# Kernel optimization log

Hardware: AMD Instinct MI355X
Metric: run time of the kernel (lower is better)

The kernel has to match this reference:

```python
import jax, jax.numpy as jnp
import numpy as np
import math

B, S, D = 2, 2048, 1024
H = 16
DK = D // H  # dim_k == dim_v == 64


def setup_inputs() -> dict:
    key = jax.random.key(0)
    ks = jax.random.split(key, 8)
    scale = 1.0 / math.sqrt(D)
    inp = {
        "query": jax.random.normal(ks[0], (B, S, D), dtype=jnp.float32),
        "key": jax.random.normal(ks[1], (B, S, D), dtype=jnp.float32),
        "value": jax.random.normal(ks[2], (B, S, D), dtype=jnp.float32),
        # stacked per-head projection weights (torch Linear y = x @ W.T; here stored as [H, D, DK])
        "Wq": jax.random.uniform(ks[3], (H, D, DK), dtype=jnp.float32, minval=-scale, maxval=scale),
        "Wk": jax.random.uniform(ks[4], (H, D, DK), dtype=jnp.float32, minval=-scale, maxval=scale),
        "Wv": jax.random.uniform(ks[5], (H, D, DK), dtype=jnp.float32, minval=-scale, maxval=scale),
        "Wo": jax.random.uniform(ks[6], (D, H * DK), dtype=jnp.float32, minval=-scale, maxval=scale),
        "bo": jax.random.uniform(ks[7], (D,), dtype=jnp.float32, minval=-scale, maxval=scale),
    }
    return inp


def reference(query, key, value, Wq, Wk, Wv, Wo, bo):
    # per-head projections, batched over heads via einsum
    q = jnp.einsum("bsd,hdk->bhsk", query, Wq)   # [B,H,S,DK]
    k = jnp.einsum("btd,hdk->bhtk", key, Wk)     # [B,H,S,DK]
    v = jnp.einsum("btd,hdv->bhtv", value, Wv)   # [B,H,S,DK]
    scores = jnp.einsum("bhsk,bhtk->bhst", q, k) / jnp.sqrt(jnp.float32(DK))
    # causal mask (is_causal=True): strictly upper triangle -> -inf
    causal = jnp.tril(jnp.ones((S, S), dtype=bool))  # True = keep
    scores = jnp.where(causal[None, None], scores, -jnp.inf)
    attn = jax.nn.softmax(scores, axis=-1)
    # NaN correction (no-op under pure causal masking, kept for faithfulness)
    attn = jnp.where(jnp.isnan(attn), 0.0, attn)
    out = jnp.einsum("bhst,bhtv->bhsv", attn, v)  # [B,H,S,DK]
    out = jnp.transpose(out, (0, 2, 1, 3)).reshape(B, S, H * DK)  # concat heads
    return out @ Wo.T + bo
```

## Files before the change

kernel.cpp:

```cpp
#include <hip/hip_runtime.h>


#define B_ 2
#define S_ 2048
#define D_ 1024
#define H_ 16
#define DK_ 64
#define NEG_BIG (-1e30f)

typedef unsigned short u16;
typedef __attribute__((ext_vector_type(8))) short bf16x8;
typedef __attribute__((ext_vector_type(4))) float f32x4;

__device__ __forceinline__ float b2f(u16 v) {
    union { unsigned u; float f; } x; x.u = ((unsigned)v) << 16; return x.f;
}
__device__ __forceinline__ u16 f2b(float f) {
    union { float f; unsigned u; } x; x.f = f;
    unsigned r = x.u + 0x7fff + ((x.u >> 16) & 1);
    return (u16)(r >> 16);
}
__device__ __forceinline__ u16 f2b_fast(float f) {
    union { float f; unsigned u; } x; x.f = f;
    return (u16)((x.u + 0x8000u) >> 16);
}

__device__ __forceinline__ bool is_f32(const void* p) {
    const unsigned* u = (const unsigned*)p;
    int cnt = 0;
#pragma unroll
    for (int i = 0; i < 64; i++) {
        unsigned e = (u[i * 8] >> 7) & 0xFFu;
        cnt += (e >= 110u && e <= 134u) ? 1 : 0;
    }
    return cnt < 32;
}

template<bool F32>
__device__ __forceinline__ bf16x8 load8(const void* p, size_t idx) {
    if constexpr (F32) {
        const float* f = (const float*)p + idx;
        float4 a = *(const float4*)f;
        float4 b = *(const float4*)(f + 4);
        bf16x8 r;
        ((u16*)&r)[0] = f2b(a.x); ((u16*)&r)[1] = f2b(a.y);
        ((u16*)&r)[2] = f2b(a.z); ((u16*)&r)[3] = f2b(a.w);
        ((u16*)&r)[4] = f2b(b.x); ((u16*)&r)[5] = f2b(b.y);
        ((u16*)&r)[6] = f2b(b.z); ((u16*)&r)[7] = f2b(b.w);
        return r;
    } else {
        return *(const bf16x8*)((const u16*)p + idx);
    }
}

__global__ __launch_bounds__(256) void wtrans(const void* Wq, const void* Wk, const void* Wv,
                                              u16* WqT, u16* WkT, u16* WvT) {
    __shared__ __align__(16) u16 Ts[64][72];
    const int t = threadIdx.x;
    const int k0 = blockIdx.x * 64;
    const int h = blockIdx.y;
    const int wsel = blockIdx.z;
    const void* W = (wsel == 0) ? Wq : (wsel == 1) ? Wk : Wv;
    u16* WT = (wsel == 0) ? WqT : (wsel == 1) ? WkT : WvT;
    const bool wf = is_f32(W);

    const int drow = t >> 2, c0 = (t & 3) * 16;
    size_t sidx = ((size_t)h * D_ + k0 + drow) * DK_ + c0;
    bf16x8 v0, v1;
    if (wf) { v0 = load8<true >(W, sidx); v1 = load8<true >(W, sidx + 8); }
    else    { v0 = load8<false>(W, sidx); v1 = load8<false>(W, sidx + 8); }
    *(bf16x8*)&Ts[drow][c0]     = v0;
    *(bf16x8*)&Ts[drow][c0 + 8] = v1;
    __syncthreads();

    const int nrow = t >> 2, kc0 = (t & 3) * 16;
    u16 tmp[16];
#pragma unroll
    for (int j = 0; j < 16; j++) tmp[j] = Ts[kc0 + j][nrow];
    u16* dst = &WT[((size_t)h * DK_ + nrow) * D_ + k0 + kc0];
    *(bf16x8*)&dst[0] = *(const bf16x8*)&tmp[0];
    *(bf16x8*)&dst[8] = *(const bf16x8*)&tmp[8];
}

template<bool AF32>
__device__ void qproj_body(const void* A, const u16* WT, u16* Qt, int bb,
                           u16 (*As)[64][72], u16 (*Wt)[64][72]) {
    const int tid = threadIdx.x, mt = blockIdx.x, h = blockIdx.y;
    const int w = tid >> 6, lane = tid & 63, quad = lane >> 4, ln = lane & 15;
    const int s0 = mt * 64;
    const int row = tid >> 3, col = (tid & 7) * 8;
    const int row1 = row + 32;
    const int brow = tid >> 2, bc0 = (tid & 3) * 16;
    const size_t wbase = ((size_t)h * DK_ + brow) * D_ + bc0;

    bf16x8 areg0, areg1, breg0, breg1;
    areg0 = load8<AF32>(A, ((size_t)bb * S_ + s0 + row ) * D_ + col);
    areg1 = load8<AF32>(A, ((size_t)bb * S_ + s0 + row1) * D_ + col);
    breg0 = *(const bf16x8*)&WT[wbase];
    breg1 = *(const bf16x8*)&WT[wbase + 8];

    f32x4 acc[4];
#pragma unroll
    for (int t = 0; t < 4; t++)
#pragma unroll
        for (int r = 0; r < 4; r++) acc[t][r] = 0.f;

    int buf = 0;
    for (int k0 = 0; k0 < D_; k0 += 64, buf ^= 1) {
        *(bf16x8*)&As[buf][row ][col] = areg0;
        *(bf16x8*)&As[buf][row1][col] = areg1;
        *(bf16x8*)&Wt[buf][brow][bc0    ] = breg0;
        *(bf16x8*)&Wt[buf][brow][bc0 + 8] = breg1;
        __syncthreads();
        if (k0 + 64 < D_) {
            areg0 = load8<AF32>(A, ((size_t)bb * S_ + s0 + row ) * D_ + k0 + 64 + col);
            areg1 = load8<AF32>(A, ((size_t)bb * S_ + s0 + row1) * D_ + k0 + 64 + col);
            breg0 = *(const bf16x8*)&WT[wbase + k0 + 64];
            breg1 = *(const bf16x8*)&WT[wbase + k0 + 64 + 8];
        }
#pragma unroll
        for (int kk = 0; kk < 2; kk++) {
            bf16x8 a = *(const bf16x8*)&As[buf][w * 16 + ln][kk * 32 + quad * 8];
#pragma unroll
            for (int t = 0; t < 4; t++) {
                bf16x8 bm = *(const bf16x8*)&Wt[buf][t * 16 + ln][kk * 32 + quad * 8];
                acc[t] = __builtin_amdgcn_mfma_f32_16x16x32_bf16(a, bm, acc[t], 0, 0, 0);
            }
        }
    }

#pragma unroll
    for (int t = 0; t < 4; t++)
#pragma unroll
        for (int r = 0; r < 4; r++)
            Qt[((size_t)bb * S_ + s0 + w * 16 + quad * 4 + r) * D_ + h * DK_ + t * 16 + ln] =
                f2b(acc[t][r] * 0.125f);
}

__global__ __launch_bounds__(256) void qproj(const void* query, const u16* WqT, u16* Qt) {
    __shared__ __align__(16) u16 As[2][64][72];
    __shared__ __align__(16) u16 Wt[2][64][72];
    const int bb = blockIdx.z;
    if (is_f32(query)) qproj_body<true >(query, WqT, Qt, bb, As, Wt);
    else               qproj_body<false>(query, WqT, Qt, bb, As, Wt);
}

template<bool AF32>
__device__ void projkv_body(const void* A, const u16* WT, u16* Ko, u16* VTo,
                            int bb, int which, u16 (*As)[64][72], u16 (*Wt)[64][72]) {
    const int tid = threadIdx.x, mt = blockIdx.x, h = blockIdx.y;
    const int w = tid >> 6, lane = tid & 63, quad = lane >> 4, ln = lane & 15;
    const int s0 = mt * 64;
    const int row = tid >> 3, col = (tid & 7) * 8;
    const int row1 = row + 32;
    const int brow = tid >> 2, bc0 = (tid & 3) * 16;
    const size_t wbase = ((size_t)h * DK_ + brow) * D_ + bc0;

    bf16x8 areg0, areg1, breg0, breg1;
    areg0 = load8<AF32>(A, ((size_t)bb * S_ + s0 + row ) * D_ + col);
    areg1 = load8<AF32>(A, ((size_t)bb * S_ + s0 + row1) * D_ + col);
    breg0 = *(const bf16x8*)&WT[wbase];
    breg1 = *(const bf16x8*)&WT[wbase + 8];

    f32x4 acc[4];
#pragma unroll
    for (int t = 0; t < 4; t++)
#pragma unroll
        for (int r = 0; r < 4; r++) acc[t][r] = 0.f;

    int buf = 0;
    for (int k0 = 0; k0 < D_; k0 += 64, buf ^= 1) {
        *(bf16x8*)&As[buf][row ][col] = areg0;
        *(bf16x8*)&As[buf][row1][col] = areg1;
        *(bf16x8*)&Wt[buf][brow][bc0    ] = breg0;
        *(bf16x8*)&Wt[buf][brow][bc0 + 8] = breg1;
        __syncthreads();
        if (k0 + 64 < D_) {
            areg0 = load8<AF32>(A, ((size_t)bb * S_ + s0 + row ) * D_ + k0 + 64 + col);
            areg1 = load8<AF32>(A, ((size_t)bb * S_ + s0 + row1) * D_ + k0 + 64 + col);
            breg0 = *(const bf16x8*)&WT[wbase + k0 + 64];
            breg1 = *(const bf16x8*)&WT[wbase + k0 + 64 + 8];
        }
#pragma unroll
        for (int kk = 0; kk < 2; kk++) {
            bf16x8 a = *(const bf16x8*)&As[buf][w * 16 + ln][kk * 32 + quad * 8];
#pragma unroll
            for (int t = 0; t < 4; t++) {
                bf16x8 bm = *(const bf16x8*)&Wt[buf][t * 16 + ln][kk * 32 + quad * 8];
                acc[t] = __builtin_amdgcn_mfma_f32_16x16x32_bf16(a, bm, acc[t], 0, 0, 0);
            }
        }
    }

    if (which == 0) {
#pragma unroll
        for (int t = 0; t < 4; t++)
#pragma unroll
            for (int r = 0; r < 4; r++)
                Ko[((size_t)h * S_ + s0 + w * 16 + quad * 4 + r) * DK_ + t * 16 + ln] =
                    f2b(acc[t][r]);
    } else {
#pragma unroll
        for (int t = 0; t < 4; t++)
#pragma unroll
            for (int r = 0; r < 4; r++)
                Wt[0][t * 16 + ln][w * 16 + quad * 4 + r] = f2b(acc[t][r]);
        __syncthreads();
        *(bf16x8*)&VTo[((size_t)h * DK_ + row ) * S_ + s0 + col] = *(const bf16x8*)&Wt[0][row ][col];
        *(bf16x8*)&VTo[((size_t)h * DK_ + row1) * S_ + s0 + col] = *(const bf16x8*)&Wt[0][row1][col];
    }
}

__global__ __launch_bounds__(256) void projkv(const void* key, const void* value,
                                              const u16* WkT, const u16* WvT,
                                              u16* KVbase, int bb) {
    __shared__ __align__(16) u16 As[2][64][72];
    __shared__ __align__(16) u16 Wt[2][64][72];
    const int which = blockIdx.z;
    const void* A = which ? value : key;
    const u16* WT = which ? WvT : WkT;
    u16* Ko  = KVbase;
    u16* VTo = KVbase + (size_t)H_ * S_ * DK_;
    if (is_f32(A)) projkv_body<true >(A, WT, Ko, VTo, bb, which, As, Wt);
    else           projkv_body<false>(A, WT, Ko, VTo, bb, which, As, Wt);
}

__global__ __launch_bounds__(512) void flashq(u16* __restrict__ Xq,
                                              const u16* __restrict__ KV,
                                              int bb0, size_t zstride) {
    __shared__ __align__(16) u16 BufA[2][64][72];
    __shared__ __align__(16) u16 BufB[2][64][72];
    __shared__ __align__(16) u16 Ps[8][16][72];
    const int tid = threadIdx.x;
    const int bx = (int)blockIdx.x;
    const int qt = (blockIdx.z & 1) ? bx : ((int)gridDim.x - 1 - bx);
    const int h = blockIdx.y;
    const int bb = bb0 + blockIdx.z;
    const u16* Kb  = KV + (size_t)blockIdx.z * zstride;
    const u16* VTb = Kb + (size_t)H_ * S_ * DK_;
    const int w = tid >> 6, lane = tid & 63, quad = lane >> 4, ln = lane & 15;
    const int half = w >> 2, wr = w & 3;
    const int s0 = qt * 128;
    const int srow = tid >> 3, scol = (tid & 7) * 8;
    const int j0max = 2 * qt;
    const int jmax  = 2 * qt + 1;
    const int jdiag = half ? jmax : j0max;

    bf16x8 kreg = *(const bf16x8*)&Kb [((size_t)h * S_  + srow) * DK_ + scol];
    bf16x8 vreg = *(const bf16x8*)&VTb[((size_t)h * DK_ + srow) * S_  + scol];

    *(bf16x8*)&BufA[0][srow][scol] = *(const bf16x8*)&Xq[((size_t)bb * S_ + s0 + srow) * D_ + h * DK_ + scol];
    *(bf16x8*)&BufA[1][srow][scol] = *(const bf16x8*)&Xq[((size_t)bb * S_ + s0 + 64 + srow) * D_ + h * DK_ + scol];
    __syncthreads();
    bf16x8 qa0 = *(const bf16x8*)&BufA[half][wr * 16 + ln][quad * 8];
    bf16x8 qa1 = *(const bf16x8*)&BufA[half][wr * 16 + ln][32 + quad * 8];
    __syncthreads();

    f32x4 O[4];
    float psum[4];
#pragma unroll
    for (int t = 0; t < 4; t++)
#pragma unroll
        for (int r = 0; r < 4; r++) O[t][r] = 0.f;
#pragma unroll
    for (int r = 0; r < 4; r++) psum[r] = 0.f;

    for (int j = 0; j <= jmax; j++) {
        const int buf = j & 1;
        *(bf16x8*)&BufA[buf][srow][scol] = kreg;
        *(bf16x8*)&BufB[buf][srow][scol] = vreg;
        __syncthreads();

        if (j < jmax) {
            kreg = *(const bf16x8*)&Kb [((size_t)h * S_  + (j + 1) * 64 + srow) * DK_ + scol];
            vreg = *(const bf16x8*)&VTb[((size_t)h * DK_ + srow) * S_ + (j + 1) * 64 + scol];
        }

        const bool act = half ? true : (j <= j0max);

        if (act) {
            f32x4 sf[4];
#pragma unroll
            for (int t = 0; t < 4; t++)
#pragma unroll
                for (int r = 0; r < 4; r++) sf[t][r] = 0.f;
#pragma unroll
            for (int kk = 0; kk < 2; kk++) {
                bf16x8 a = kk ? qa1 : qa0;
#pragma unroll
                for (int t = 0; t < 4; t++) {
                    bf16x8 bm = *(const bf16x8*)&BufA[buf][t * 16 + ln][kk * 32 + quad * 8];
                    sf[t] = __builtin_amdgcn_mfma_f32_16x16x32_bf16(a, bm, sf[t], 0, 0, 0);
                }
            }
            if (j == jdiag) {
#pragma unroll
                for (int t = 0; t < 4; t++) {
                    int keyl = t * 16 + ln;
#pragma unroll
                    for (int r = 0; r < 4; r++) {
                        int qr = wr * 16 + quad * 4 + r;
                        if (keyl > qr) sf[t][r] = NEG_BIG;
                    }
                }
            }
#pragma unroll
            for (int t = 0; t < 4; t++)
#pragma unroll
                for (int r = 0; r < 4; r++) {
                    float p = __expf(sf[t][r]);
                    psum[r] += p;
                    Ps[w][quad * 4 + r][t * 16 + ln] = f2b_fast(p);
                }
        }
        __syncthreads();

        if (act) {
#pragma unroll
            for (int kk = 0; kk < 2; kk++) {
                bf16x8 a = *(const bf16x8*)&Ps[w][ln][kk * 32 + quad * 8];
#pragma unroll
                for (int t = 0; t < 4; t++) {
                    bf16x8 bm = *(const bf16x8*)&BufB[buf][t * 16 + ln][kk * 32 + quad * 8];
                    O[t] = __builtin_amdgcn_mfma_f32_16x16x32_bf16(a, bm, O[t], 0, 0, 0);
                }
            }
        }
    }

#pragma unroll
    for (int r = 0; r < 4; r++) {
        float s = psum[r];
        s += __shfl_xor(s, 1, 64);
        s += __shfl_xor(s, 2, 64);
        s += __shfl_xor(s, 4, 64);
        s += __shfl_xor(s, 8, 64);
        float inv = 1.0f / s;
        int sr = s0 + half * 64 + wr * 16 + quad * 4 + r;
#pragma unroll
        for (int t = 0; t < 4; t++) {
            Xq[((size_t)bb * S_ + sr) * D_ + h * DK_ + t * 16 + ln] = f2b(O[t][r] * inv);
        }
    }
}

__global__ __launch_bounds__(256) void copyx(const u16* __restrict__ src,
                                             u16* __restrict__ dst) {
    size_t i = ((size_t)blockIdx.x * 256 + threadIdx.x) * 8;
    *(bf16x8*)&dst[i] = *(const bf16x8*)&src[i];
}

template<bool WF32>
__device__ void outgemm_body(const u16* X, const void* Wo, const void* bo, bool bf32,
                             float* Y, u16 (*As)[64][72], u16 (*Bs)[64][72]) {
    const int tid = threadIdx.x, mt = blockIdx.x, nt = blockIdx.y;
    const int w = tid >> 6, lane = tid & 63, quad = lane >> 4, ln = lane & 15;
    const int m0 = mt * 64, n0 = nt * 64;
    const int row = tid >> 3, col = (tid & 7) * 8;
    const int row1 = row + 32;

    bf16x8 areg0, areg1, wreg0, wreg1;
    areg0 = *(const bf16x8*)&X[(size_t)(m0 + row ) * D_ + col];
    areg1 = *(const bf16x8*)&X[(size_t)(m0 + row1) * D_ + col];
    wreg0 = load8<WF32>(Wo, (size_t)(n0 + row ) * D_ + col);
    wreg1 = load8<WF32>(Wo, (size_t)(n0 + row1) * D_ + col);

    f32x4 acc[4];
#pragma unroll
    for (int t = 0; t < 4; t++)
#pragma unroll
        for (int r = 0; r < 4; r++) acc[t][r] = 0.f;

    int buf = 0;
    for (int k0 = 0; k0 < D_; k0 += 64, buf ^= 1) {
        *(bf16x8*)&As[buf][row ][col] = areg0;
        *(bf16x8*)&As[buf][row1][col] = areg1;
        *(bf16x8*)&Bs[buf][row ][col] = wreg0;
        *(bf16x8*)&Bs[buf][row1][col] = wreg1;
        __syncthreads();
        if (k0 + 64 < D_) {
            areg0 = *(const bf16x8*)&X[(size_t)(m0 + row ) * D_ + k0 + 64 + col];
            areg1 = *(const bf16x8*)&X[(size_t)(m0 + row1) * D_ + k0 + 64 + col];
            wreg0 = load8<WF32>(Wo, (size_t)(n0 + row ) * D_ + k0 + 64 + col);
            wreg1 = load8<WF32>(Wo, (size_t)(n0 + row1) * D_ + k0 + 64 + col);
        }
#pragma unroll
        for (int kk = 0; kk < 2; kk++) {
            bf16x8 a = *(const bf16x8*)&As[buf][w * 16 + ln][kk * 32 + quad * 8];
#pragma unroll
            for (int t = 0; t < 4; t++) {
                bf16x8 bm = *(const bf16x8*)&Bs[buf][t * 16 + ln][kk * 32 + quad * 8];
                acc[t] = __builtin_amdgcn_mfma_f32_16x16x32_bf16(a, bm, acc[t], 0, 0, 0);
            }
        }
    }

#pragma unroll
    for (int t = 0; t < 4; t++) {
        int n = n0 + t * 16 + ln;
        float bias = bf32 ? ((const float*)bo)[n] : b2f(((const u16*)bo)[n]);
#pragma unroll
        for (int r = 0; r < 4; r++) {
            int m = m0 + w * 16 + quad * 4 + r;
            Y[(size_t)m * D_ + n] = acc[t][r] + bias;
        }
    }
}

__global__ __launch_bounds__(256) void outgemm(const u16* __restrict__ X,
                                               const void* Wo, const void* bo,
                                               float* __restrict__ Y) {
    __shared__ __align__(16) u16 As[2][64][72];
    __shared__ __align__(16) u16 Bs[2][64][72];
    const bool wf = is_f32(Wo), bf = is_f32(bo);
    if (wf) outgemm_body<true >(X, Wo, bo, bf, Y, As, Bs);
    else    outgemm_body<false>(X, Wo, bo, bf, Y, As, Bs);
}

extern "C" void kernel_launch(void* const* d_in, const int* in_sizes, int n_in,
                              void* d_out, int out_size, void* d_ws, size_t ws_size,
                              hipStream_t stream) {
    const void* q  = d_in[0];
    const void* k  = d_in[1];
    const void* v  = d_in[2];
    const void* Wq = d_in[3];
    const void* Wk = d_in[4];
    const void* Wv = d_in[5];
    const void* Wo = d_in[6];
    const void* bo = d_in[7];

    u16* ob   = (u16*)d_out;
    u16* Xq   = ob;
    u16* WkT  = ob + (size_t)4 * 1024 * 1024;
    u16* WvT  = WkT + (size_t)1024 * 1024;
    u16* WqT  = WvT + (size_t)1024 * 1024;
    u16* ws16 = (u16*)d_ws;
    const size_t kvblk = (size_t)2 * H_ * S_ * DK_;
    const bool bigws = ws_size >= (size_t)16 * 1024 * 1024;

    wtrans<<<dim3(D_ / 64, H_, 3), dim3(256), 0, stream>>>(Wq, Wk, Wv, WqT, WkT, WvT);
    qproj<<<dim3(S_ / 64, H_, B_), dim3(256), 0, stream>>>(q, WqT, Xq);
    if (bigws) {
        projkv<<<dim3(S_ / 64, H_, 2), dim3(256), 0, stream>>>(k, v, WkT, WvT, ws16, 0);
        projkv<<<dim3(S_ / 64, H_, 2), dim3(256), 0, stream>>>(k, v, WkT, WvT, ws16 + kvblk, 1);
        flashq<<<dim3(S_ / 128, H_, 2), dim3(512), 0, stream>>>(Xq, ws16, 0, kvblk);
    } else {
        projkv<<<dim3(S_ / 64, H_, 2), dim3(256), 0, stream>>>(k, v, WkT, WvT, ws16, 0);
        flashq<<<dim3(S_ / 128, H_, 1), dim3(512), 0, stream>>>(Xq, ws16, 0, 0);
        projkv<<<dim3(S_ / 64, H_, 2), dim3(256), 0, stream>>>(k, v, WkT, WvT, ws16, 1);
        flashq<<<dim3(S_ / 128, H_, 1), dim3(512), 0, stream>>>(Xq, ws16, 1, 0);
    }
    copyx<<<dim3((B_ * S_ * D_) / (256 * 8)), dim3(256), 0, stream>>>(Xq, ws16);
    outgemm<<<dim3((B_ * S_) / 64, D_ / 64), dim3(256), 0, stream>>>(ws16, Wo, bo, (float*)d_out);
}
```

Measured before the change: 271.9 us.

## Pre-convert Wo to bf16 and use LDS-direct double-buffered output GEMM

When the workspace is large, the output projection now uses a new 512-thread GEMM with 128x64 tiles. It loads tiles straight from global memory into LDS with XOR-swizzled addressing and double buffering. Wo is converted to bf16 once, inside the existing copy kernel, so the GEMM inner loop no longer converts weights. This targets the cost of register-staged loads and per-tile fp32 conversion. In exchange it adds workspace use for the bf16 Wo and a larger shared-memory footprint per block.

```diff
diff --git a/kernel.cpp b/kernel.cpp
--- a/kernel.cpp
+++ b/kernel.cpp
@@ -23,6 +23,12 @@
 __device__ __forceinline__ u16 f2b_fast(float f) {
     union { float f; unsigned u; } x; x.f = f;
     return (u16)((x.u + 0x8000u) >> 16);
+}
+
+__device__ __forceinline__ void gload16(const void* g, void* l) {
+    __builtin_amdgcn_global_load_lds(
+        (const __attribute__((address_space(1))) void*)g,
+        (__attribute__((address_space(3))) void*)l, 16, 0, 0);
 }
 
 __device__ __forceinline__ bool is_f32(const void* p) {
@@ -344,10 +350,83 @@
     }
 }
 
+__global__ __launch_bounds__(256) void copyx2(const u16* __restrict__ src,
+                                              u16* __restrict__ dst,
+                                              const void* Wo, u16* WoB) {
+    const int b = (int)blockIdx.x;
+    if (b < 4096) {
+        size_t i = ((size_t)b * 256 + threadIdx.x) * 8;
+        *(bf16x8*)&dst[i] = *(const bf16x8*)&src[i];
+    } else {
+        size_t i = ((size_t)(b - 4096) * 256 + threadIdx.x) * 8;
+        if (is_f32(Wo)) *(bf16x8*)&WoB[i] = load8<true >(Wo, i);
+        else            *(bf16x8*)&WoB[i] = load8<false>(Wo, i);
+    }
+}
+
 __global__ __launch_bounds__(256) void copyx(const u16* __restrict__ src,
                                              u16* __restrict__ dst) {
     size_t i = ((size_t)blockIdx.x * 256 + threadIdx.x) * 8;
     *(bf16x8*)&dst[i] = *(const bf16x8*)&src[i];
+}
+
+__global__ __launch_bounds__(512) void outgemm2(const u16* __restrict__ X,
+                                                const u16* __restrict__ WoB,
+                                                const void* bo,
+                                                float* __restrict__ Y) {
+    __shared__ __align__(16) u16 AsL[2][128 * 64];
+    __shared__ __align__(16) u16 BsL[2][64 * 64];
+    const int tid = threadIdx.x;
+    const int m0 = blockIdx.x * 128, n0 = blockIdx.y * 64;
+    const int w = tid >> 6, lane = tid & 63, quad = lane >> 4, ln = lane & 15;
+    const int lr = lane >> 3;
+    const int lc = (lane & 7) ^ lr;
+    const bool bf = is_f32(bo);
+
+    const int ar0 = (w * 2 + 0) * 8 + lr;
+    const int ar1 = (w * 2 + 1) * 8 + lr;
+    const int brw = w * 8 + lr;
+
+    f32x4 acc[4];
+#pragma unroll
+    for (int t = 0; t < 4; t++)
+#pragma unroll
+        for (int r = 0; r < 4; r++) acc[t][r] = 0.f;
+
+    gload16(&X  [(size_t)(m0 + ar0) * D_ + lc * 8], &AsL[0][(w * 2 + 0) * 512]);
+    gload16(&X  [(size_t)(m0 + ar1) * D_ + lc * 8], &AsL[0][(w * 2 + 1) * 512]);
+    gload16(&WoB[(size_t)(n0 + brw) * D_ + lc * 8], &BsL[0][w * 512]);
+
+    int buf = 0;
+    for (int k0 = 0; k0 < D_; k0 += 64, buf ^= 1) {
+        __syncthreads();
+        if (k0 + 64 < D_) {
+            gload16(&X  [(size_t)(m0 + ar0) * D_ + k0 + 64 + lc * 8], &AsL[buf ^ 1][(w * 2 + 0) * 512]);
+            gload16(&X  [(size_t)(m0 + ar1) * D_ + k0 + 64 + lc * 8], &AsL[buf ^ 1][(w * 2 + 1) * 512]);
+            gload16(&WoB[(size_t)(n0 + brw) * D_ + k0 + 64 + lc * 8], &BsL[buf ^ 1][w * 512]);
+        }
+#pragma unroll
+        for (int kk = 0; kk < 2; kk++) {
+            const int rc = ((kk * 4 + quad) ^ (ln & 7)) * 8;
+            bf16x8 a = *(const bf16x8*)&AsL[buf][(w * 16 + ln) * 64 + rc];
+#pragma unroll
+            for (int t = 0; t < 4; t++) {
+                bf16x8 bm = *(const bf16x8*)&BsL[buf][(t * 16 + ln) * 64 + rc];
+                acc[t] = __builtin_amdgcn_mfma_f32_16x16x32_bf16(a, bm, acc[t], 0, 0, 0);
+            }
+        }
+    }
+
+#pragma unroll
+    for (int t = 0; t < 4; t++) {
+        int n = n0 + t * 16 + ln;
+        float bias = bf ? ((const float*)bo)[n] : b2f(((const u16*)bo)[n]);
+#pragma unroll
+        for (int r = 0; r < 4; r++) {
+            int m = m0 + w * 16 + quad * 4 + r;
+            Y[(size_t)m * D_ + n] = acc[t][r] + bias;
+        }
+    }
 }
 
 template<bool WF32>
@@ -436,6 +515,7 @@
     u16* WqT  = WvT + (size_t)1024 * 1024;
     u16* ws16 = (u16*)d_ws;
     const size_t kvblk = (size_t)2 * H_ * S_ * DK_;
+    u16* WoB = ws16 + kvblk;
     const bool bigws = ws_size >= (size_t)16 * 1024 * 1024;
 
     wtrans<<<dim3(D_ / 64, H_, 3), dim3(256), 0, stream>>>(Wq, Wk, Wv, WqT, WkT, WvT);
@@ -444,12 +524,14 @@
         projkv<<<dim3(S_ / 64, H_, 2), dim3(256), 0, stream>>>(k, v, WkT, WvT, ws16, 0);
         projkv<<<dim3(S_ / 64, H_, 2), dim3(256), 0, stream>>>(k, v, WkT, WvT, ws16 + kvblk, 1);
         flashq<<<dim3(S_ / 128, H_, 2), dim3(512), 0, stream>>>(Xq, ws16, 0, kvblk);
+        copyx2<<<dim3(4096 + 512), dim3(256), 0, stream>>>(Xq, ws16, Wo, WoB);
+        outgemm2<<<dim3((B_ * S_) / 128, D_ / 64), dim3(512), 0, stream>>>(ws16, WoB, bo, (float*)d_out);
     } else {
         projkv<<<dim3(S_ / 64, H_, 2), dim3(256), 0, stream>>>(k, v, WkT, WvT, ws16, 0);
         flashq<<<dim3(S_ / 128, H_, 1), dim3(512), 0, stream>>>(Xq, ws16, 0, 0);
         projkv<<<dim3(S_ / 64, H_, 2), dim3(256), 0, stream>>>(k, v, WkT, WvT, ws16, 1);
         flashq<<<dim3(S_ / 128, H_, 1), dim3(512), 0, stream>>>(Xq, ws16, 1, 0);
-    }
-    copyx<<<dim3((B_ * S_ * D_) / (256 * 8)), dim3(256), 0, stream>>>(Xq, ws16);
-    outgemm<<<dim3((B_ * S_) / 64, D_ / 64), dim3(256), 0, stream>>>(ws16, Wo, bo, (float*)d_out);
-}
+        copyx<<<dim3((B_ * S_ * D_) / (256 * 8)), dim3(256), 0, stream>>>(Xq, ws16);
+        outgemm<<<dim3((B_ * S_) / 64, D_ / 64), dim3(256), 0, stream>>>(ws16, Wo, bo, (float*)d_out);
+    }
+}
```

Result: faster. 263.8 us (-3.0%).
